# Optimization experiments

Measured on AMD Instinct MI355X. Metric: run time of the kernel, lower is better.

The kernel has to match this reference:

```python
import jax, jax.numpy as jnp
import numpy as np

B, S, D_MODEL, D_K, D_V = 8, 2048, 1024, 512, 512


def setup_inputs() -> dict:
    key = jax.random.key(0)
    ks = jax.random.split(key, 7)
    sq = jax.random.normal(ks[0], (B, S, D_MODEL), dtype=jnp.float32)
    skv = jax.random.normal(ks[1], (B, S, D_MODEL), dtype=jnp.float32)
    q_pad = jax.random.uniform(ks[2], (B, S)) < 0.1
    kv_pad = jax.random.uniform(ks[3], (B, S)) < 0.1
    Wq = jax.random.normal(ks[4], (D_MODEL, D_K), dtype=jnp.float32) * (D_MODEL ** -0.5)
    Wk = jax.random.normal(ks[5], (D_MODEL, D_K), dtype=jnp.float32) * (D_MODEL ** -0.5)
    Wv = jax.random.normal(ks[6], (D_MODEL, D_V), dtype=jnp.float32) * (D_MODEL ** -0.5)
    return {
        "source_query": sq,
        "source_key_value": skv,
        "source_query_padding_mask": q_pad,
        "source_key_value_padding_mask": kv_pad,
        "Wq": Wq,
        "Wk": Wk,
        "Wv": Wv,
    }


def reference(source_query, source_key_value, source_query_padding_mask,
              source_key_value_padding_mask, Wq, Wk, Wv):
    neg_inf = jnp.float32(-jnp.inf)
    q = source_query @ Wq          # [B,Sq,d_k]
    k = source_key_value @ Wk      # [B,Sk,d_k]
    v = source_key_value @ Wv      # [B,Sk,d_v]
    scale = jnp.float32(D_K) ** -0.5
    scores = jnp.einsum("bqd,bkd->bqk", q, k) * scale  # [B,Sq,Sk]
    # query padding mask broadcast along key dim, kv padding mask along query dim
    pad = source_query_padding_mask[:, :, None] | source_key_value_padding_mask[:, None, :]
    scores = jnp.where(pad, neg_inf, scores)
    # causal mask (masked=True): positions above diagonal blocked
    Sq = scores.shape[1]
    causal = jnp.tril(jnp.ones((Sq, Sq), dtype=bool))
    scores = jnp.where(causal[None, :, :], scores, neg_inf)
    attn = jax.nn.softmax(scores, axis=-1)
    # fully-masked rows produce NaN -> zero (matches torch nan masked_fill)
    attn = jnp.where(jnp.isnan(attn), jnp.float32(0.0), attn)
    # dropout p=0.0 (eval): identity
    out = jnp.einsum("bqk,bkv->bqv", attn, v)  # [B,Sq,d_v]
    return out
```

## Files before the change

kernel.cpp:

```cpp
#include <hip/hip_runtime.h>

typedef unsigned short u16;
typedef unsigned int   u32;
typedef __attribute__((ext_vector_type(4))) float  f32x4;
typedef __attribute__((ext_vector_type(8))) __bf16 bf16x8;

#define BATCH 8
#define SEQ   2048
#define DMODEL 1024
#define DK    512
#define DV    512
#define SCALE 0.044194173824159216f

__device__ __forceinline__ u16 f2bf(float f) {
  u32 u = __float_as_uint(f);
  return (u16)((u + 0x7fffu + ((u >> 16) & 1u)) >> 16);
}

__device__ __forceinline__ bool read_mask(const void* p, int idx, int mode) {
  if (mode == 1) return ((const unsigned char*)p)[idx] != 0;
  if (mode == 2) return ((const float*)p)[idx] != 0.0f;
  return ((const int*)p)[idx] != 0;
}

__device__ __forceinline__ void gl_lds16(const u16* g, u16* l) {
  __builtin_amdgcn_global_load_lds(
      (const __attribute__((address_space(1))) u32*)g,
      (__attribute__((address_space(3))) u32*)l, 16, 0, 0);
}

__global__ void detect_mode(const int* __restrict__ qp, int* __restrict__ flag) {
  __shared__ int f;
  if (threadIdx.x == 0) f = 0;
  __syncthreads();
  int local = 0;
  for (int i = threadIdx.x; i < 4096; i += 256) {
    int v = qp[i];
    if (v == 0x3F800000) local |= 2;
    else if (v != 0 && v != 1 && v != -1) local |= 1;
  }
  if (local) atomicOr(&f, local);
  __syncthreads();
  if (threadIdx.x == 0) {
    int m = 0;
    if (f & 2) m = 2; else if (f & 1) m = 1;
    *flag = m;
  }
}

__global__ __launch_bounds__(256) void wt_transpose(const float* __restrict__ W0,
                                                    const float* __restrict__ W1,
                                                    const float* __restrict__ W2,
                                                    u16* __restrict__ dst) {
  const float* W = (blockIdx.z == 0) ? W0 : (blockIdx.z == 1) ? W1 : W2;
  u16* out = dst + (size_t)blockIdx.z * (DK * DMODEL);
  __shared__ float T[32][33];
  int k0 = blockIdx.x * 32, n0 = blockIdx.y * 32;
  int tx = threadIdx.x, ty = threadIdx.y;
#pragma unroll
  for (int i = 0; i < 4; ++i) {
    int r = ty + i * 8;
    T[r][tx] = W[(size_t)(k0 + r) * DK + n0 + tx];
  }
  __syncthreads();
#pragma unroll
  for (int i = 0; i < 4; ++i) {
    int r = ty + i * 8;
    out[(size_t)(n0 + r) * DMODEL + k0 + tx] = f2bf(T[tx][r]);
  }
}

__global__ __launch_bounds__(256) void convert_bf16(const float* __restrict__ src,
                                                    u16* __restrict__ dst) {
  int i = (blockIdx.x * 256 + threadIdx.x) * 8;
  f32x4 a = *(const f32x4*)(src + i);
  f32x4 b = *(const f32x4*)(src + i + 4);
  uint4 o;
  o.x = (u32)f2bf(a[0]) | ((u32)f2bf(a[1]) << 16);
  o.y = (u32)f2bf(a[2]) | ((u32)f2bf(a[3]) << 16);
  o.z = (u32)f2bf(b[0]) | ((u32)f2bf(b[1]) << 16);
  o.w = (u32)f2bf(b[2]) | ((u32)f2bf(b[3]) << 16);
  *(uint4*)(dst + i) = o;
}

__global__ __launch_bounds__(256, 3) void proj_gemm(const u16* __restrict__ A,
                                                    const u16* __restrict__ Wt_base,
                                                    int z0, u16* __restrict__ dst0,
                                                    u16* __restrict__ dst1) {
  int z = z0 + blockIdx.z;
  const u16* Wt = Wt_base + (size_t)z * (DK * DMODEL);
  u16* dst = (z == 2) ? dst1 : dst0;
  int n0 = blockIdx.x * 128, m0 = blockIdx.y * 128;

  __shared__ __align__(16) u16 As[128 * 64];
  __shared__ __align__(16) u16 Bs[128 * 64];

  int tid = threadIdx.x, lane = tid & 63, w = tid >> 6;
  int wm = w & 1, wn = w >> 1;
  int l15 = lane & 15, lg = lane >> 4;
  int r3 = lane >> 3, c7 = lane & 7;
  int csw = c7 ^ r3;

  f32x4 acc[4][4];
#pragma unroll
  for (int m = 0; m < 4; ++m)
#pragma unroll
    for (int n = 0; n < 4; ++n) acc[m][n] = (f32x4)0.0f;

  for (int k0 = 0; k0 < DMODEL; k0 += 64) {
    __syncthreads();
#pragma unroll
    for (int u = 0; u < 4; ++u) {
      int t = w * 4 + u;
      gl_lds16(A  + (size_t)(m0 + t * 8 + r3) * DMODEL + k0 + csw * 8, &As[t * 512]);
      gl_lds16(Wt + (size_t)(n0 + t * 8 + r3) * DMODEL + k0 + csw * 8, &Bs[t * 512]);
    }
    __syncthreads();
#pragma unroll
    for (int ks = 0; ks < 2; ++ks) {
      bf16x8 af[4], bfv[4];
#pragma unroll
      for (int m = 0; m < 4; ++m) {
        int row = wm * 64 + m * 16 + l15;
        af[m] = *(const bf16x8*)&As[row * 64 + (((ks * 4 + lg) ^ (l15 & 7)) * 8)];
      }
#pragma unroll
      for (int n = 0; n < 4; ++n) {
        int row = wn * 64 + n * 16 + l15;
        bfv[n] = *(const bf16x8*)&Bs[row * 64 + (((ks * 4 + lg) ^ (l15 & 7)) * 8)];
      }
#pragma unroll
      for (int m = 0; m < 4; ++m)
#pragma unroll
        for (int n = 0; n < 4; ++n)
          acc[m][n] = __builtin_amdgcn_mfma_f32_16x16x32_bf16(af[m], bfv[n], acc[m][n], 0, 0, 0);
    }
  }

  if (z != 2) {
#pragma unroll
    for (int m = 0; m < 4; ++m) {
      int rowb = m0 + wm * 64 + m * 16;
#pragma unroll
      for (int n = 0; n < 4; ++n) {
        int col = n0 + wn * 64 + n * 16 + l15;
        size_t base = (size_t)(rowb >> 4) * 8192 + (size_t)(col >> 5) * 512 + (col & 31);
#pragma unroll
        for (int r = 0; r < 4; ++r)
          dst[base + (lg * 4 + r) * 32] = f2bf(acc[m][n][r]);
      }
    }
  } else {
#pragma unroll
    for (int m = 0; m < 4; ++m) {
      int row0 = m0 + wm * 64 + m * 16 + lg * 4;
      int b = row0 >> 11, s0 = row0 & 2047;
#pragma unroll
      for (int n = 0; n < 4; ++n) {
        int dv = n0 + wn * 64 + n * 16 + l15;
        size_t off = (size_t)b * (SEQ * DV) + (size_t)(dv >> 4) * 32768 +
                     (size_t)(s0 >> 5) * 512 + (dv & 15) * 32 + (s0 & 31);
        u16 tmp[4] __attribute__((aligned(8)));
#pragma unroll
        for (int r = 0; r < 4; ++r) tmp[r] = f2bf(acc[m][n][r]);
        *(uint2*)&dst[off] = *(const uint2*)tmp;
      }
    }
  }
}

__global__ __launch_bounds__(1024, 4) void attn_kernel(
    const u16* __restrict__ Qf, const u16* __restrict__ Kf,
    const u16* __restrict__ Vf, const void* __restrict__ qpad,
    const void* __restrict__ kvpad, const int* __restrict__ flag,
    float* __restrict__ out) {
  __shared__ __align__(16) u16 Qs[32 * 512];
  __shared__ __align__(16) u16 Pbuf[32 * 136];
  __shared__ __align__(16) float partm[32 * 8];
  __shared__ __align__(16) float partl[32 * 8];

  int tid = threadIdx.x;
  int lane = tid & 63, w = tid >> 6;
  int l15 = lane & 15, lg = lane >> 4;
  int wk = w & 7;
  int mS = w >> 3;
  int mf = w & 1;
  int dq = w >> 1;
  int bi = blockIdx.x;
  int b = bi & 7, c = bi >> 3;
  int mode = *flag;
  int lanoff = l15 * 32 + lg * 8;

  const u16* Qb = Qf + (size_t)b * (SEQ * DK);
  const u16* Kb = Kf + (size_t)b * (SEQ * DK);
  const u16* Vb = Vf + (size_t)b * (SEQ * DV);

#pragma unroll 1
  for (int pass = 0; pass < 2; ++pass) {
    int qt = pass ? c : (63 - c);
    int q0 = qt * 32;

    {
      const u16* qsrc = Qb + (size_t)qt * 16384 + lane * 8;
#pragma unroll
      for (int u = 0; u < 2; ++u) {
        int i = w * 2 + u;
        gl_lds16(qsrc + i * 512, &Qs[i * 512]);
      }
    }

    f32x4 o[4];
#pragma unroll
    for (int n = 0; n < 4; ++n) o[n] = (f32x4)0.0f;

    float mo[2][4], lsum[4];
#pragma unroll
    for (int mfi = 0; mfi < 2; ++mfi)
#pragma unroll
      for (int r = 0; r < 4; ++r) mo[mfi][r] = -1e38f;
#pragma unroll
    for (int r = 0; r < 4; ++r) lsum[r] = 0.0f;

    int nkt = (q0 + 159) >> 7;
    __syncthreads();

    for (int kt = 0; kt < nkt; ++kt) {
      int k0 = kt << 7;
      int key = k0 + wk * 16 + l15;
      bool kvm = read_mask(kvpad, b * SEQ + key, mode);

      f32x4 sa = (f32x4)0.0f, sb = (f32x4)0.0f;
      {
        const u16* kp = Kb + (size_t)(kt * 8 + wk) * 8192 + lanoff;
        const u16* qp = &Qs[mS * 8192 + lanoff];
#pragma unroll
        for (int ks = 0; ks < 16; ks += 2) {
          bf16x8 qv0 = *(const bf16x8*)(qp + ks * 512);
          bf16x8 kv0 = *(const bf16x8*)(kp + ks * 512);
          bf16x8 qv1 = *(const bf16x8*)(qp + (ks + 1) * 512);
          bf16x8 kv1 = *(const bf16x8*)(kp + (ks + 1) * 512);
          sa = __builtin_amdgcn_mfma_f32_16x16x32_bf16(qv0, kv0, sa, 0, 0, 0);
          sb = __builtin_amdgcn_mfma_f32_16x16x32_bf16(qv1, kv1, sb, 0, 0, 0);
        }
      }

      float sv[4];
#pragma unroll
      for (int r = 0; r < 4; ++r) {
        int qrow = q0 + mS * 16 + lg * 4 + r;
        float x = (sa[r] + sb[r]) * SCALE;
        sv[r] = (kvm || key > qrow) ? -__builtin_inff() : x;
      }

      float wmax[4];
#pragma unroll
      for (int r = 0; r < 4; ++r) wmax[r] = sv[r];
#pragma unroll
      for (int d = 1; d < 16; d <<= 1)
#pragma unroll
        for (int r = 0; r < 4; ++r) wmax[r] = fmaxf(wmax[r], __shfl_xor(wmax[r], d));
      if (l15 == 0) {
#pragma unroll
        for (int r = 0; r < 4; ++r) partm[(mS * 16 + lg * 4 + r) * 8 + wk] = wmax[r];
      }
      __syncthreads();

      float al[2][4];
#pragma unroll
      for (int mfi = 0; mfi < 2; ++mfi)
#pragma unroll
        for (int r = 0; r < 4; ++r) {
          int row = mfi * 16 + lg * 4 + r;
          f32x4 p0 = *(const f32x4*)&partm[row * 8];
          f32x4 p1 = *(const f32x4*)&partm[row * 8 + 4];
          float tm = fmaxf(fmaxf(fmaxf(p0[0], p0[1]), fmaxf(p0[2], p0[3])),
                           fmaxf(fmaxf(p1[0], p1[1]), fmaxf(p1[2], p1[3])));
          float mn = fmaxf(mo[mfi][r], fmaxf(tm, -1e38f));
          al[mfi][r] = __expf(mo[mfi][r] - mn);
          mo[mfi][r] = mn;
        }
      float ws[4];
#pragma unroll
      for (int r = 0; r < 4; ++r) {
        int row = mS * 16 + lg * 4 + r;
        float mS_m = mS ? mo[1][r] : mo[0][r];
        float p = __expf(sv[r] - mS_m);
        Pbuf[row * 136 + wk * 16 + l15] = f2bf(p);
        ws[r] = p;
      }
#pragma unroll
      for (int d = 1; d < 16; d <<= 1)
#pragma unroll
        for (int r = 0; r < 4; ++r) ws[r] += __shfl_xor(ws[r], d);
#pragma unroll
      for (int r = 0; r < 4; ++r) {
        float alS = mS ? al[1][r] : al[0][r];
        lsum[r] = lsum[r] * alS + ws[r];
      }
      __syncthreads();

#pragma unroll
      for (int n = 0; n < 4; ++n)
#pragma unroll
        for (int r = 0; r < 4; ++r) {
          float alF = mf ? al[1][r] : al[0][r];
          o[n][r] *= alF;
        }

      {
        bf16x8 pa[4];
#pragma unroll
        for (int ks = 0; ks < 4; ++ks)
          pa[ks] = *(const bf16x8*)&Pbuf[(mf * 16 + l15) * 136 + ks * 32 + lg * 8];
        const u16* vp = Vb + (size_t)(dq * 4) * 32768 + (size_t)(kt * 4) * 512 + lanoff;
#pragma unroll
        for (int n = 0; n < 4; ++n) {
#pragma unroll
          for (int ks = 0; ks < 4; ++ks) {
            bf16x8 bv = *(const bf16x8*)(vp + (size_t)n * 32768 + ks * 512);
            o[n] = __builtin_amdgcn_mfma_f32_16x16x32_bf16(pa[ks], bv, o[n], 0, 0, 0);
          }
        }
      }
    }

    if (l15 == 0) {
#pragma unroll
      for (int r = 0; r < 4; ++r) partl[(mS * 16 + lg * 4 + r) * 8 + wk] = lsum[r];
    }
    __syncthreads();
    {
      float f[4];
#pragma unroll
      for (int r = 0; r < 4; ++r) {
        int row = mf * 16 + lg * 4 + r;
        f32x4 a = *(const f32x4*)&partl[row * 8];
        f32x4 b2 = *(const f32x4*)&partl[row * 8 + 4];
        float l = (a[0] + a[1] + a[2] + a[3]) + (b2[0] + b2[1] + b2[2] + b2[3]);
        bool qp = read_mask(qpad, b * SEQ + q0 + row, mode);
        f[r] = (l > 0.0f && !qp) ? 1.0f / l : 0.0f;
      }
#pragma unroll
      for (int n = 0; n < 4; ++n) {
        int dv = dq * 64 + n * 16 + l15;
#pragma unroll
        for (int r = 0; r < 4; ++r) {
          int row = mf * 16 + lg * 4 + r;
          out[(size_t)(b * SEQ + q0 + row) * DV + dv] = o[n][r] * f[r];
        }
      }
    }
    __syncthreads();
  }
}

extern "C" void kernel_launch(void* const* d_in, const int* in_sizes, int n_in,
                              void* d_out, int out_size, void* d_ws, size_t ws_size,
                              hipStream_t stream) {
  const float* sq  = (const float*)d_in[0];
  const float* skv = (const float*)d_in[1];
  const void* qp   = d_in[2];
  const void* kvp  = d_in[3];
  const float* Wq  = (const float*)d_in[4];
  const float* Wk  = (const float*)d_in[5];
  const float* Wv  = (const float*)d_in[6];
  char* ws = (char*)d_ws;

  u16* Abf = (u16*)ws;
  u16* Qf  = (u16*)(ws + 33554432);
  u16* Kf  = (u16*)(ws + 50331648);
  u16* Vf  = (u16*)(ws + 67108864);
  u16* Wt  = (u16*)(ws + 83886080);
  int* flag = (int*)(ws + 87031808);

  wt_transpose<<<dim3(32, 16, 3), dim3(32, 8, 1), 0, stream>>>(Wq, Wk, Wv, Wt);
  detect_mode<<<1, 256, 0, stream>>>((const int*)qp, flag);

  convert_bf16<<<8192, 256, 0, stream>>>(sq, Abf);
  proj_gemm<<<dim3(4, 128, 1), dim3(256), 0, stream>>>(Abf, Wt, 0, Qf, Qf);

  convert_bf16<<<8192, 256, 0, stream>>>(skv, Abf);
  proj_gemm<<<dim3(4, 128, 2), dim3(256), 0, stream>>>(Abf, Wt, 1, Kf, Vf);

  attn_kernel<<<dim3(256), dim3(1024), 0, stream>>>(Qf, Kf, Vf, qp, kvp, flag,
                                                    (float*)d_out);
}
```

Before: 459.8 us.

## Halve attention query tile to 16 rows with 512 blocks and swizzled Q LDS

The attention kernel now processes 16 query rows per block with 8 waves instead of 32 rows with 16 waves, launching 512 blocks of 512 threads. Each wave owns one 16-key slice for the score MFMA and one 64-column output slice for PV, which removes the split row-group bookkeeping. Q staging in shared memory uses an XOR swizzle to reduce bank conflicts. More blocks improves occupancy and load balance across CUs, but each K/V tile is now reloaded for only 16 query rows, which doubles global K/V traffic per query.

Result: faster. 403.6 us (-12.2%).

```diff
diff --git a/kernel.cpp b/kernel.cpp
--- a/kernel.cpp
+++ b/kernel.cpp
@@ -169,27 +169,25 @@
   }
 }
 
-__global__ __launch_bounds__(1024, 4) void attn_kernel(
+__global__ __launch_bounds__(512, 4) void attn_kernel(
     const u16* __restrict__ Qf, const u16* __restrict__ Kf,
     const u16* __restrict__ Vf, const void* __restrict__ qpad,
     const void* __restrict__ kvpad, const int* __restrict__ flag,
     float* __restrict__ out) {
-  __shared__ __align__(16) u16 Qs[32 * 512];
-  __shared__ __align__(16) u16 Pbuf[32 * 136];
-  __shared__ __align__(16) float partm[32 * 8];
-  __shared__ __align__(16) float partl[32 * 8];
+  __shared__ __align__(16) u16 Qs[16 * 512];
+  __shared__ __align__(16) u16 Pbuf[16 * 136];
+  __shared__ __align__(16) float partm[16 * 8];
+  __shared__ __align__(16) float partl[16 * 8];
 
   int tid = threadIdx.x;
   int lane = tid & 63, w = tid >> 6;
   int l15 = lane & 15, lg = lane >> 4;
-  int wk = w & 7;
-  int mS = w >> 3;
-  int mf = w & 1;
-  int dq = w >> 1;
   int bi = blockIdx.x;
   int b = bi & 7, c = bi >> 3;
   int mode = *flag;
   int lanoff = l15 * 32 + lg * 8;
+  int qswz = (((l15 * 4 + lg) ^ (l15 >> 1)) * 8);
+  int sswz = ((lane ^ ((lane >> 3) & 7)) * 8);
 
   const u16* Qb = Qf + (size_t)b * (SEQ * DK);
   const u16* Kb = Kf + (size_t)b * (SEQ * DK);
@@ -197,11 +195,11 @@
 
 #pragma unroll 1
   for (int pass = 0; pass < 2; ++pass) {
-    int qt = pass ? c : (63 - c);
-    int q0 = qt * 32;
+    int qt = pass ? c : (127 - c);
+    int q0 = qt * 16;
 
     {
-      const u16* qsrc = Qb + (size_t)qt * 16384 + lane * 8;
+      const u16* qsrc = Qb + (size_t)qt * 8192 + sswz;
 #pragma unroll
       for (int u = 0; u < 2; ++u) {
         int i = w * 2 + u;
@@ -213,31 +211,25 @@
 #pragma unroll
     for (int n = 0; n < 4; ++n) o[n] = (f32x4)0.0f;
 
-    float mo[2][4], lsum[4];
-#pragma unroll
-    for (int mfi = 0; mfi < 2; ++mfi)
-#pragma unroll
-      for (int r = 0; r < 4; ++r) mo[mfi][r] = -1e38f;
-#pragma unroll
-    for (int r = 0; r < 4; ++r) lsum[r] = 0.0f;
-
-    int nkt = (q0 + 159) >> 7;
+    float mo[4], lsum[4];
+#pragma unroll
+    for (int r = 0; r < 4; ++r) { mo[r] = -1e38f; lsum[r] = 0.0f; }
+
+    int nkt = (q0 + 143) >> 7;
     __syncthreads();
 
     for (int kt = 0; kt < nkt; ++kt) {
-      int k0 = kt << 7;
-      int key = k0 + wk * 16 + l15;
+      int key = (kt << 7) + w * 16 + l15;
       bool kvm = read_mask(kvpad, b * SEQ + key, mode);
 
       f32x4 sa = (f32x4)0.0f, sb = (f32x4)0.0f;
       {
-        const u16* kp = Kb + (size_t)(kt * 8 + wk) * 8192 + lanoff;
-        const u16* qp = &Qs[mS * 8192 + lanoff];
+        const u16* kp = Kb + (size_t)(kt * 8 + w) * 8192 + lanoff;
 #pragma unroll
         for (int ks = 0; ks < 16; ks += 2) {
-          bf16x8 qv0 = *(const bf16x8*)(qp + ks * 512);
+          bf16x8 qv0 = *(const bf16x8*)&Qs[ks * 512 + qswz];
           bf16x8 kv0 = *(const bf16x8*)(kp + ks * 512);
-          bf16x8 qv1 = *(const bf16x8*)(qp + (ks + 1) * 512);
+          bf16x8 qv1 = *(const bf16x8*)&Qs[(ks + 1) * 512 + qswz];
           bf16x8 kv1 = *(const bf16x8*)(kp + (ks + 1) * 512);
           sa = __builtin_amdgcn_mfma_f32_16x16x32_bf16(qv0, kv0, sa, 0, 0, 0);
           sb = __builtin_amdgcn_mfma_f32_16x16x32_bf16(qv1, kv1, sb, 0, 0, 0);
@@ -247,7 +239,7 @@
       float sv[4];
 #pragma unroll
       for (int r = 0; r < 4; ++r) {
-        int qrow = q0 + mS * 16 + lg * 4 + r;
+        int qrow = q0 + lg * 4 + r;
         float x = (sa[r] + sb[r]) * SCALE;
         sv[r] = (kvm || key > qrow) ? -__builtin_inff() : x;
       }
@@ -261,31 +253,23 @@
         for (int r = 0; r < 4; ++r) wmax[r] = fmaxf(wmax[r], __shfl_xor(wmax[r], d));
       if (l15 == 0) {
 #pragma unroll
-        for (int r = 0; r < 4; ++r) partm[(mS * 16 + lg * 4 + r) * 8 + wk] = wmax[r];
+        for (int r = 0; r < 4; ++r) partm[(lg * 4 + r) * 8 + w] = wmax[r];
       }
       __syncthreads();
 
-      float al[2][4];
-#pragma unroll
-      for (int mfi = 0; mfi < 2; ++mfi)
-#pragma unroll
-        for (int r = 0; r < 4; ++r) {
-          int row = mfi * 16 + lg * 4 + r;
-          f32x4 p0 = *(const f32x4*)&partm[row * 8];
-          f32x4 p1 = *(const f32x4*)&partm[row * 8 + 4];
-          float tm = fmaxf(fmaxf(fmaxf(p0[0], p0[1]), fmaxf(p0[2], p0[3])),
-                           fmaxf(fmaxf(p1[0], p1[1]), fmaxf(p1[2], p1[3])));
-          float mn = fmaxf(mo[mfi][r], fmaxf(tm, -1e38f));
-          al[mfi][r] = __expf(mo[mfi][r] - mn);
-          mo[mfi][r] = mn;
-        }
-      float ws[4];
+      float al[4], ws[4];
 #pragma unroll
       for (int r = 0; r < 4; ++r) {
-        int row = mS * 16 + lg * 4 + r;
-        float mS_m = mS ? mo[1][r] : mo[0][r];
-        float p = __expf(sv[r] - mS_m);
-        Pbuf[row * 136 + wk * 16 + l15] = f2bf(p);
+        int row = lg * 4 + r;
+        f32x4 p0 = *(const f32x4*)&partm[row * 8];
+        f32x4 p1 = *(const f32x4*)&partm[row * 8 + 4];
+        float tm = fmaxf(fmaxf(fmaxf(p0[0], p0[1]), fmaxf(p0[2], p0[3])),
+                         fmaxf(fmaxf(p1[0], p1[1]), fmaxf(p1[2], p1[3])));
+        float mn = fmaxf(mo[r], fmaxf(tm, -1e38f));
+        al[r] = __expf(mo[r] - mn);
+        mo[r] = mn;
+        float p = __expf(sv[r] - mn);
+        Pbuf[row * 136 + w * 16 + l15] = f2bf(p);
         ws[r] = p;
       }
 #pragma unroll
@@ -293,26 +277,20 @@
 #pragma unroll
         for (int r = 0; r < 4; ++r) ws[r] += __shfl_xor(ws[r], d);
 #pragma unroll
-      for (int r = 0; r < 4; ++r) {
-        float alS = mS ? al[1][r] : al[0][r];
-        lsum[r] = lsum[r] * alS + ws[r];
-      }
+      for (int r = 0; r < 4; ++r) lsum[r] = lsum[r] * al[r] + ws[r];
       __syncthreads();
 
 #pragma unroll
       for (int n = 0; n < 4; ++n)
 #pragma unroll
-        for (int r = 0; r < 4; ++r) {
-          float alF = mf ? al[1][r] : al[0][r];
-          o[n][r] *= alF;
-        }
+        for (int r = 0; r < 4; ++r) o[n][r] *= al[r];
 
       {
         bf16x8 pa[4];
 #pragma unroll
         for (int ks = 0; ks < 4; ++ks)
-          pa[ks] = *(const bf16x8*)&Pbuf[(mf * 16 + l15) * 136 + ks * 32 + lg * 8];
-        const u16* vp = Vb + (size_t)(dq * 4) * 32768 + (size_t)(kt * 4) * 512 + lanoff;
+          pa[ks] = *(const bf16x8*)&Pbuf[l15 * 136 + ks * 32 + lg * 8];
+        const u16* vp = Vb + (size_t)(w * 4) * 32768 + (size_t)(kt * 4) * 512 + lanoff;
 #pragma unroll
         for (int n = 0; n < 4; ++n) {
 #pragma unroll
@@ -326,14 +304,14 @@
 
     if (l15 == 0) {
 #pragma unroll
-      for (int r = 0; r < 4; ++r) partl[(mS * 16 + lg * 4 + r) * 8 + wk] = lsum[r];
+      for (int r = 0; r < 4; ++r) partl[(lg * 4 + r) * 8 + w] = lsum[r];
     }
     __syncthreads();
     {
       float f[4];
 #pragma unroll
       for (int r = 0; r < 4; ++r) {
-        int row = mf * 16 + lg * 4 + r;
+        int row = lg * 4 + r;
         f32x4 a = *(const f32x4*)&partl[row * 8];
         f32x4 b2 = *(const f32x4*)&partl[row * 8 + 4];
         float l = (a[0] + a[1] + a[2] + a[3]) + (b2[0] + b2[1] + b2[2] + b2[3]);
@@ -342,10 +320,10 @@
       }
 #pragma unroll
       for (int n = 0; n < 4; ++n) {
-        int dv = dq * 64 + n * 16 + l15;
+        int dv = w * 64 + n * 16 + l15;
 #pragma unroll
         for (int r = 0; r < 4; ++r) {
-          int row = mf * 16 + lg * 4 + r;
+          int row = lg * 4 + r;
           out[(size_t)(b * SEQ + q0 + row) * DV + dv] = o[n][r] * f[r];
         }
       }
@@ -382,6 +360,6 @@
   convert_bf16<<<8192, 256, 0, stream>>>(skv, Abf);
   proj_gemm<<<dim3(4, 128, 2), dim3(256), 0, stream>>>(Abf, Wt, 1, Kf, Vf);
 
-  attn_kernel<<<dim3(256), dim3(1024), 0, stream>>>(Qf, Kf, Vf, qp, kvp, flag,
-                                                    (float*)d_out);
-}
+  attn_kernel<<<dim3(512), dim3(512), 0, stream>>>(Qf, Kf, Vf, qp, kvp, flag,
+                                                   (float*)d_out);
+}
```
